# Kernel tuning notes

Measured on AMD Instinct MI355X. Metric: run time of the kernel, lower is better.

The kernel has to match this reference:

```python
import jax, jax.numpy as jnp
import numpy as np
import math

B, S, D = 4, 4096, 1024
H = 16
HD = D // H          # head_dim = 64
M = 256              # nb_features (random projection dim)


def _orthogonal_gaussian(key, m, d):
    # FAVOR+ orthogonal random features: blocks of d orthogonal rows,
    # each row rescaled to a chi-distributed norm (norm of a d-dim gaussian).
    n_blocks = int(math.ceil(m / d))
    keys = jax.random.split(key, n_blocks + 1)
    blocks = []
    for i in range(n_blocks):
        g = jax.random.normal(keys[i], (d, d), dtype=jnp.float32)
        q, _ = jnp.linalg.qr(g)
        blocks.append(q.T)
    W = jnp.concatenate(blocks, axis=0)[:m]  # [m, d]
    norms = jnp.linalg.norm(
        jax.random.normal(keys[-1], (m, d), dtype=jnp.float32), axis=1, keepdims=True)
    return W * norms


def _softmax_kernel(x, proj, is_query, eps=1e-4):
    # x: [b,h,s,d]; proj: [m,d]. Standard FAVOR+ positive softmax features.
    d = x.shape[-1]
    ratio = proj.shape[0] ** -0.5
    x = x * (d ** -0.25)
    u = jnp.einsum('bhsd,md->bhsm', x, proj)  # projection
    diag = 0.5 * jnp.sum(x * x, axis=-1, keepdims=True)  # [b,h,s,1]
    if is_query:
        stab = jnp.max(u, axis=-1, keepdims=True)
    else:
        stab = jnp.max(u, axis=(-1, -2), keepdims=True)
    return ratio * (jnp.exp(u - diag - stab) + eps)


def performer_attention(Q, K, V, mask, proj):
    # Q,K,V: [b,h,s,d], mask: [b,s]
    scale = HD ** -0.25
    m4 = mask[:, None, :, None]
    Qs = Q * scale
    Ks = K * scale * m4
    Vs = V * m4
    q_prime = _softmax_kernel(Qs, proj, is_query=True)   # [b,h,s,m]
    k_prime = _softmax_kernel(Ks, proj, is_query=False)  # [b,h,s,m]
    # linear attention: O(s*m*d)
    kv = jnp.einsum('bhsm,bhsd->bhmd', k_prime, Vs)      # [b,h,m,d]
    z = 1.0 / (jnp.einsum('bhsm,bhm->bhs', q_prime, jnp.sum(k_prime, axis=2)) + 1e-6)
    out = jnp.einsum('bhsm,bhmd->bhsd', q_prime, kv) * z[..., None]
    return out


def setup_inputs() -> dict:
    key = jax.random.key(0)
    ks = jax.random.split(key, 9)
    X = jax.random.normal(ks[0], (B, S, D), dtype=jnp.float32)
    mask = jnp.ones((B, S), dtype=jnp.float32)
    s = D ** -0.5
    Wq = jax.random.normal(ks[1], (D, D), dtype=jnp.float32) * s
    bq = jnp.zeros((D,), dtype=jnp.float32)
    Wk = jax.random.normal(ks[2], (D, D), dtype=jnp.float32) * s
    bk = jnp.zeros((D,), dtype=jnp.float32)
    Wv = jax.random.normal(ks[3], (D, D), dtype=jnp.float32) * s
    bv = jnp.zeros((D,), dtype=jnp.float32)
    proj = _orthogonal_gaussian(ks[4], M, HD)
    return {"X": X, "mask": mask, "Wq": Wq, "bq": bq, "Wk": Wk, "bk": bk,
            "Wv": Wv, "bv": bv, "proj": proj}


def _split_heads(x):
    b, s, _ = x.shape
    return x.reshape(b, s, H, HD).transpose(0, 2, 1, 3)


def reference(X, mask, Wq, bq, Wk, bk, Wv, bv, proj):
    Q = _split_heads(X @ Wq + bq)
    K = _split_heads(X @ Wk + bk)
    V = _split_heads(X @ Wv + bv)
    attn = performer_attention(Q, K, V, mask, proj)  # [b,h,s,hd]
    out = attn.transpose(0, 2, 1, 3).reshape(B, S, D)
    return out
```

## Files before the change

### kernel.cpp

```cpp
#include <hip/hip_runtime.h>
#include <stdint.h>

#define DEVI static __device__ __forceinline__

typedef unsigned short u16;
typedef unsigned int u32;
typedef __attribute__((ext_vector_type(8))) short short8;
typedef __attribute__((ext_vector_type(4))) float f32x4;
typedef __attribute__((ext_vector_type(4))) unsigned short ushort4_t;

#define BB 4
#define SS 4096
#define DD 1024
#define HH 16
#define HDD 64
#define MM 256
#define BHN 64

DEVI u16 f2bf(float f) {
    u32 u = __float_as_uint(f);
    u += 0x7fffu + ((u >> 16) & 1u);
    return (u16)(u >> 16);
}
DEVI float bf2f(u16 h) { return __uint_as_float(((u32)h) << 16); }
DEVI u32 fenc(float f) {
    u32 u = __float_as_uint(f);
    return (u & 0x80000000u) ? ~u : (u | 0x80000000u);
}
DEVI float fdec(u32 k) {
    u32 u = (k & 0x80000000u) ? (k & 0x7fffffffu) : ~k;
    return __uint_as_float(u);
}

typedef __attribute__((address_space(1))) const unsigned int as1_u32;
typedef __attribute__((address_space(3))) unsigned int as3_u32;
DEVI void load_lds16(const void* g, void* lds) {
    __builtin_amdgcn_global_load_lds((as1_u32*)g, (as3_u32*)lds, 16, 0, 0);
}


__global__ void conv_bf16(const float* __restrict__ src, u16* __restrict__ dst, int n4) {
    int i = blockIdx.x * 256 + threadIdx.x;
    if (i < n4) {
        float4 v = reinterpret_cast<const float4*>(src)[i];
        ushort4_t o = { f2bf(v.x), f2bf(v.y), f2bf(v.z), f2bf(v.w) };
        reinterpret_cast<ushort4_t*>(dst)[i] = o;
    }
}

__global__ void conv_w(const float* __restrict__ Wq, const float* __restrict__ Wk,
                       const float* __restrict__ Wv, u16* __restrict__ Wt) {
    __shared__ float tile[64][65];
    const int jt = blockIdx.x, kt = blockIdx.y;
    const float* src = (jt < 16) ? Wq : (jt < 32) ? Wk : Wv;
    const int j0 = (jt & 15) * 64, k0 = kt * 64;
    const int t = threadIdx.x;
    for (int i = 0; i < 16; ++i) {
        int lin = t + i * 256;
        int kl = lin >> 6, jl = lin & 63;
        tile[kl][jl] = src[(size_t)(k0 + kl) * DD + j0 + jl];
    }
    __syncthreads();
    const int jg0 = jt * 64;
    for (int i = 0; i < 16; ++i) {
        int lin = t + i * 256;
        int jl = lin >> 6, kl = lin & 63;
        Wt[(size_t)(jg0 + jl) * DD + k0 + kl] = f2bf(tile[kl][jl]);
    }
}

__global__ __launch_bounds__(512, 2) void gemm1_k32(
    const u16* __restrict__ Xbf, const u16* __restrict__ Wt,
    const float* __restrict__ bq, const float* __restrict__ bk, const float* __restrict__ bv,
    const float* __restrict__ mask,
    u16* __restrict__ Qh, u16* __restrict__ Kh, u16* __restrict__ Vt,
    float* __restrict__ dq, float* __restrict__ dk)
{
    extern __shared__ __align__(16) char smem[];
    const int tid = threadIdx.x, l = tid & 63, wv = tid >> 6;
    const int wm = wv >> 2, wn = wv & 3;
    const int bid = blockIdx.x;
    const int xcd = bid & 7, i6 = bid >> 3;
    const int bx = xcd * 8 + i6 / 12, by = i6 % 12;
    const int row0 = bx * 256, col0 = by * 256;

    int sA[2];
#pragma unroll
    for (int j = 0; j < 2; ++j) {
        const int o = j * 8192 + tid * 16;
        const int R = o >> 7;
        const int logpos = (o & 127) ^ ((R & 7) << 4);
        const int r = 2 * R + (logpos >> 6);
        const int c8 = (logpos >> 4) & 3;
        sA[j] = r * DD + c8 * 8;
    }
    const size_t xbase = (size_t)row0 * DD;
    const size_t wbase = (size_t)col0 * DD;

    #define ABUF(b) ((char*)smem + (b) * 16384)
    #define BBUF(b) ((char*)smem + 65536 + (b) * 16384)
    #define STA(b, kt, j) load_lds16(Xbf + xbase + (kt) * 32 + sA[j], ABUF(b) + (j) * 8192 + wv * 1024)
    #define STB(b, kt, j) load_lds16(Wt + wbase + (kt) * 32 + sA[j], BBUF(b) + (j) * 8192 + wv * 1024)

#pragma unroll
    for (int t = 0; t < 3; ++t) { STA(t, t, 0); STA(t, t, 1); STB(t, t, 0); STB(t, t, 1); }
    asm volatile("s_waitcnt vmcnt(8)" ::: "memory");
    __builtin_amdgcn_s_barrier();
    __builtin_amdgcn_sched_barrier(0);

    f32x4 acc[8][4] = {};
    const int hl = (l & 15) >> 1;
    const int xorc = hl << 4;
    const int pa = ((wm * 64 + hl) * 128 + (l & 1) * 64 + (l >> 4) * 16) ^ xorc;
    const int pb = ((wn * 32 + hl) * 128 + (l & 1) * 64 + (l >> 4) * 16) ^ xorc;

    for (int kt = 0; kt < 32; ++kt) {
        const int p = kt & 3, pn = (kt + 3) & 3;
        const bool more = (kt + 3) < 32;
        short8 bfr[4];
#pragma unroll
        for (int q = 0; q < 4; ++q) {
            if (more) {
                if (q == 0)      STA(pn, kt + 3, 0);
                else if (q == 1) STA(pn, kt + 3, 1);
                else if (q == 2) STB(pn, kt + 3, 0);
                else             STB(pn, kt + 3, 1);
            }
            if (q == 0) {
#pragma unroll
                for (int nf = 0; nf < 4; ++nf)
                    bfr[nf] = *(const short8*)(BBUF(p) + pb + nf * 1024);
            }
            short8 a[2];
#pragma unroll
            for (int i = 0; i < 2; ++i)
                a[i] = *(const short8*)(ABUF(p) + pa + (q * 2 + i) * 1024);
            __builtin_amdgcn_s_setprio(1);
#pragma unroll
            for (int i = 0; i < 2; ++i)
#pragma unroll
                for (int nf = 0; nf < 4; ++nf)
                    acc[q * 2 + i][nf] = __builtin_amdgcn_mfma_f32_16x16x32_bf16(a[i], bfr[nf], acc[q * 2 + i][nf], 0, 0, 0);
            __builtin_amdgcn_s_setprio(0);
        }
        if (kt < 31) {
            if (kt + 3 < 32)      asm volatile("s_waitcnt vmcnt(8)" ::: "memory");
            else if (kt + 2 < 32) asm volatile("s_waitcnt vmcnt(4)" ::: "memory");
            else                  asm volatile("s_waitcnt vmcnt(0)" ::: "memory");
            __builtin_amdgcn_s_barrier();
            __builtin_amdgcn_sched_barrier(0);
        }
    }

    const int region = by >> 2;
    const int h = ((by & 3) << 2) + wn;
    const int rg = row0 + wm * 128;
    const int b = rg >> 12;
    const int sb = rg & 4095;
    const size_t bh = (size_t)(b * HH + h);
    const int dd = l & 15;
    const int jbase = ((by & 3) << 8) + wn * 64;

    if (region == 0) {
        float bias[4];
#pragma unroll
        for (int nf = 0; nf < 4; ++nf) bias[nf] = bq[jbase + nf * 16 + dd];
#pragma unroll
        for (int mf = 0; mf < 8; ++mf) {
            float ds4[4];
#pragma unroll
            for (int g = 0; g < 4; ++g) {
                const int s = sb + mf * 16 + ((l >> 4) << 2) + g;
                float dsum = 0.f;
#pragma unroll
                for (int nf = 0; nf < 4; ++nf) {
                    u16 hv = f2bf((acc[mf][nf][g] + bias[nf]) * 0.125f);
                    Qh[(bh * SS + s) * HDD + nf * 16 + dd] = hv;
                    float fv = bf2f(hv);
                    dsum += fv * fv;
                }
                dsum += __shfl_xor(dsum, 1);
                dsum += __shfl_xor(dsum, 2);
                dsum += __shfl_xor(dsum, 4);
                dsum += __shfl_xor(dsum, 8);
                ds4[g] = 0.5f * dsum;
            }
            if (dd == 0)
                *(float4*)(dq + bh * SS + sb + mf * 16 + ((l >> 4) << 2)) =
                    make_float4(ds4[0], ds4[1], ds4[2], ds4[3]);
        }
    } else if (region == 1) {
        float bias[4];
#pragma unroll
        for (int nf = 0; nf < 4; ++nf) bias[nf] = bk[jbase + nf * 16 + dd];
#pragma unroll
        for (int mf = 0; mf < 8; ++mf) {
            float ds4[4];
#pragma unroll
            for (int g = 0; g < 4; ++g) {
                const int s = sb + mf * 16 + ((l >> 4) << 2) + g;
                const float m = mask[b * SS + s];
                float dsum = 0.f;
#pragma unroll
                for (int nf = 0; nf < 4; ++nf) {
                    u16 hv = f2bf((acc[mf][nf][g] + bias[nf]) * m * 0.125f);
                    Kh[(bh * SS + s) * HDD + nf * 16 + dd] = hv;
                    float fv = bf2f(hv);
                    dsum += fv * fv;
                }
                dsum += __shfl_xor(dsum, 1);
                dsum += __shfl_xor(dsum, 2);
                dsum += __shfl_xor(dsum, 4);
                dsum += __shfl_xor(dsum, 8);
                ds4[g] = 0.5f * dsum;
            }
            if (dd == 0)
                *(float4*)(dk + bh * SS + sb + mf * 16 + ((l >> 4) << 2)) =
                    make_float4(ds4[0], ds4[1], ds4[2], ds4[3]);
        }
    } else {
        float bias[4];
#pragma unroll
        for (int nf = 0; nf < 4; ++nf) bias[nf] = bv[jbase + nf * 16 + dd];
#pragma unroll
        for (int mf = 0; mf < 8; ++mf) {
            const int s0 = sb + mf * 16 + ((l >> 4) << 2);
#pragma unroll
            for (int nf = 0; nf < 4; ++nf) {
                ushort4_t pk;
#pragma unroll
                for (int g = 0; g < 4; ++g) {
                    const float m = mask[b * SS + s0 + g];
                    pk[g] = f2bf((acc[mf][nf][g] + bias[nf]) * m);
                }
                *(ushort4_t*)(Vt + (bh * HDD + nf * 16 + dd) * SS + s0) = pk;
            }
        }
    }
    #undef ABUF
    #undef BBUF
    #undef STA
    #undef STB
}

__global__ __launch_bounds__(256, 2) void stab_kernel(
    const u16* __restrict__ Kh, const u16* __restrict__ projb, u32* __restrict__ stabkey)
{
    __shared__ __align__(16) u16 Klds[64 * 64];
    __shared__ float red4[4];
    const int tid = threadIdx.x, l = tid & 63, wv = tid >> 6;
    const int rt = blockIdx.x, bh = blockIdx.y;
    short8 pb[4][2];
#pragma unroll
    for (int nf = 0; nf < 4; ++nf)
#pragma unroll
        for (int ks = 0; ks < 2; ++ks)
            pb[nf][ks] = *(const short8*)(projb + (wv * 64 + nf * 16 + (l & 15)) * HDD + ks * 32 + (l >> 4) * 8);
    const size_t sbase = (size_t)bh * SS + rt * 64;
#pragma unroll
    for (int c = 0; c < 2; ++c) {
        const int rb = wv * 16 + c * 8;
        const int r = rb + (l >> 3);
        load_lds16(Kh + (sbase + r) * HDD + (((l & 7) ^ (r & 7)) * 8), (char*)Klds + rb * 128);
    }
    __syncthreads();
    float mx = -3.0e38f;
#pragma unroll
    for (int sf = 0; sf < 4; ++sf) {
        const int s = sf * 16 + (l & 15);
        f32x4 u4[4] = {};
#pragma unroll
        for (int ks = 0; ks < 2; ++ks) {
            short8 ak = *(const short8*)((const char*)Klds + s * 128 + ((ks * 64 + (l >> 4) * 16) ^ ((s & 7) << 4)));
#pragma unroll
            for (int nf = 0; nf < 4; ++nf)
                u4[nf] = __builtin_amdgcn_mfma_f32_16x16x32_bf16(ak, pb[nf][ks], u4[nf], 0, 0, 0);
        }
#pragma unroll
        for (int nf = 0; nf < 4; ++nf)
#pragma unroll
            for (int g = 0; g < 4; ++g) mx = fmaxf(mx, u4[nf][g]);
    }
#pragma unroll
    for (int o = 1; o < 64; o <<= 1) mx = fmaxf(mx, __shfl_xor(mx, o));
    if (l == 0) red4[wv] = mx;
    __syncthreads();
    if (tid == 0) {
        float m2 = fmaxf(fmaxf(red4[0], red4[1]), fmaxf(red4[2], red4[3]));
        atomicMax(stabkey + bh, fenc(m2));
    }
}

__global__ __launch_bounds__(256, 2) void kv_fused(
    const u16* __restrict__ Kh, const u16* __restrict__ Vt,
    const u16* __restrict__ projb, const float* __restrict__ dk,
    const u32* __restrict__ stabkey,
    float* __restrict__ kv_part, float* __restrict__ ksum_part)
{
    __shared__ __align__(16) u16 Klds[64 * 64];
    __shared__ __align__(16) u16 Vlds[64 * 64];
    __shared__ __align__(16) u16 Kp[256 * 64];
    const int tid = threadIdx.x, l = tid & 63, wv = tid >> 6;
    const int ck = blockIdx.x, bh = blockIdx.y;
    const float stab = fdec(stabkey[bh]);
    short8 pb[4][2];
#pragma unroll
    for (int nf = 0; nf < 4; ++nf)
#pragma unroll
        for (int ks = 0; ks < 2; ++ks)
            pb[nf][ks] = *(const short8*)(projb + (wv * 64 + nf * 16 + (l & 15)) * HDD + ks * 32 + (l >> 4) * 8);
    f32x4 acc[4][4] = {};
    float ksc[4] = {0.f, 0.f, 0.f, 0.f};
    const size_t sbase = (size_t)bh * SS + ck * 512;
    for (int it = 0; it < 8; ++it) {
        const int s0 = it * 64;
#pragma unroll
        for (int c = 0; c < 2; ++c) {
            const int rb = wv * 16 + c * 8;
            const int r = rb + (l >> 3);
            const int sc = ((l & 7) ^ (r & 7)) * 8;
            load_lds16(Kh + (sbase + s0 + r) * HDD + sc, (char*)Klds + rb * 128);
            load_lds16(Vt + ((size_t)bh * HDD + r) * SS + ck * 512 + s0 + sc, (char*)Vlds + rb * 128);
        }
        __syncthreads();
#pragma unroll
        for (int sf = 0; sf < 4; ++sf) {
            const int s = sf * 16 + (l & 15);
            f32x4 u4[4] = {};
#pragma unroll
            for (int ks = 0; ks < 2; ++ks) {
                short8 ak = *(const short8*)((const char*)Klds + s * 128 + ((ks * 64 + (l >> 4) * 16) ^ ((s & 7) << 4)));
#pragma unroll
                for (int nf = 0; nf < 4; ++nf)
                    u4[nf] = __builtin_amdgcn_mfma_f32_16x16x32_bf16(ak, pb[nf][ks], u4[nf], 0, 0, 0);
            }
            const int srow = sf * 16 + (l >> 4) * 4;
            const float4 dkv = *(const float4*)(dk + sbase + s0 + srow);
#pragma unroll
            for (int nf = 0; nf < 4; ++nf) {
                const int m = wv * 64 + nf * 16 + (l & 15);
                u16 h0 = f2bf(0.0625f * (__expf(u4[nf][0] - dkv.x - stab) + 1e-4f));
                u16 h1 = f2bf(0.0625f * (__expf(u4[nf][1] - dkv.y - stab) + 1e-4f));
                u16 h2 = f2bf(0.0625f * (__expf(u4[nf][2] - dkv.z - stab) + 1e-4f));
                u16 h3 = f2bf(0.0625f * (__expf(u4[nf][3] - dkv.w - stab) + 1e-4f));
                ksc[nf] += bf2f(h0) + bf2f(h1) + bf2f(h2) + bf2f(h3);
                uint2 w; w.x = (u32)h0 | ((u32)h1 << 16); w.y = (u32)h2 | ((u32)h3 << 16);
                *(uint2*)((char*)Kp + m * 128 + ((srow * 2) ^ ((m & 7) << 4))) = w;
            }
        }
#pragma unroll
        for (int ks = 0; ks < 2; ++ks) {
            short8 am[4], bv8[4];
#pragma unroll
            for (int mf = 0; mf < 4; ++mf) {
                const int m = wv * 64 + mf * 16 + (l & 15);
                am[mf] = *(const short8*)((const char*)Kp + m * 128 + ((ks * 64 + (l >> 4) * 16) ^ ((m & 7) << 4)));
            }
#pragma unroll
            for (int nf = 0; nf < 4; ++nf) {
                const int d = nf * 16 + (l & 15);
                bv8[nf] = *(const short8*)((const char*)Vlds + d * 128 + ((ks * 64 + (l >> 4) * 16) ^ ((d & 7) << 4)));
            }
#pragma unroll
            for (int mf = 0; mf < 4; ++mf)
#pragma unroll
                for (int nf = 0; nf < 4; ++nf)
                    acc[mf][nf] = __builtin_amdgcn_mfma_f32_16x16x32_bf16(am[mf], bv8[nf], acc[mf][nf], 0, 0, 0);
        }
        __syncthreads();
    }
    const size_t pbase = (size_t)ck * BHN + bh;
#pragma unroll
    for (int nf = 0; nf < 4; ++nf) {
        float v = ksc[nf];
        v += __shfl_xor(v, 16);
        v += __shfl_xor(v, 32);
        if (l < 16) ksum_part[pbase * MM + wv * 64 + nf * 16 + l] = v;
    }
#pragma unroll
    for (int mf = 0; mf < 4; ++mf)
#pragma unroll
        for (int nf = 0; nf < 4; ++nf)
            *(f32x4*)(kv_part + (pbase * HDD + nf * 16 + (l & 15)) * MM + wv * 64 + mf * 16 + (l >> 4) * 4) = acc[mf][nf];
}

__global__ void reduceB2(const float* __restrict__ kv_part, const float* __restrict__ ksum_part,
                         u16* __restrict__ Bmat) {
    const int bh = blockIdx.x, n = blockIdx.y, t = threadIdx.x;
    float s = 0.f;
    if (n < 64) {
#pragma unroll
        for (int ck = 0; ck < 8; ++ck) s += kv_part[(((size_t)ck * BHN + bh) * HDD + n) * MM + t];
    } else if (n == 64) {
#pragma unroll
        for (int ck = 0; ck < 8; ++ck) s += ksum_part[((size_t)ck * BHN + bh) * MM + t];
    }
    Bmat[((size_t)bh * 80 + n) * MM + t] = (n <= 64) ? f2bf(s) : (u16)0;
}

__global__ __launch_bounds__(256, 2) void out_fused(
    const u16* __restrict__ Qh, const u16* __restrict__ projb,
    const float* __restrict__ dq, const u16* __restrict__ Bmat,
    float* __restrict__ out)
{
    __shared__ __align__(16) u16 Blds[80 * 256];
    __shared__ __align__(16) u16 Qlds[32 * 64];
    __shared__ __align__(16) u16 qlds[32 * 256];
    __shared__ float red[4][32];
    const int tid = threadIdx.x, l = tid & 63, wv = tid >> 6;
    const int rt = blockIdx.x, bh = blockIdx.y;
#pragma unroll
    for (int c = 0; c < 10; ++c) {
        const int r = (wv * 10 + c) * 2 + (l >> 5);
        load_lds16(Bmat + (size_t)bh * 20480 + r * 256 + (((l & 31) ^ (r & 7)) * 8),
                   (char*)Blds + (wv * 10 + c) * 1024);
    }
    const size_t srowbase = (size_t)bh * SS + rt * 32;
    {
        const int rb = wv * 8;
        const int r = rb + (l >> 3);
        load_lds16(Qh + (srowbase + r) * HDD + (((l & 7) ^ (r & 7)) * 8), (char*)Qlds + rb * 128);
    }
    short8 pa[4][2];
#pragma unroll
    for (int mf = 0; mf < 4; ++mf)
#pragma unroll
        for (int ks = 0; ks < 2; ++ks)
            pa[mf][ks] = *(const short8*)(projb + (wv * 64 + mf * 16 + (l & 15)) * HDD + ks * 32 + (l >> 4) * 8);
    __syncthreads();
    f32x4 u[4][2] = {};
#pragma unroll
    for (int ks = 0; ks < 2; ++ks) {
        short8 bq8[2];
#pragma unroll
        for (int nf = 0; nf < 2; ++nf) {
            const int s = nf * 16 + (l & 15);
            bq8[nf] = *(const short8*)((const char*)Qlds + s * 128 + ((ks * 64 + (l >> 4) * 16) ^ ((s & 7) << 4)));
        }
#pragma unroll
        for (int mf = 0; mf < 4; ++mf)
#pragma unroll
            for (int nf = 0; nf < 2; ++nf)
                u[mf][nf] = __builtin_amdgcn_mfma_f32_16x16x32_bf16(pa[mf][ks], bq8[nf], u[mf][nf], 0, 0, 0);
    }
#pragma unroll
    for (int nf = 0; nf < 2; ++nf) {
        float v = -3.0e38f;
#pragma unroll
        for (int mf = 0; mf < 4; ++mf)
#pragma unroll
            for (int g = 0; g < 4; ++g) v = fmaxf(v, u[mf][nf][g]);
        v = fmaxf(v, __shfl_xor(v, 16));
        v = fmaxf(v, __shfl_xor(v, 32));
        if ((l >> 4) == 0) red[wv][nf * 16 + l] = v;
    }
    __syncthreads();
#pragma unroll
    for (int nf = 0; nf < 2; ++nf) {
        const int s = nf * 16 + (l & 15);
        const float mx = fmaxf(fmaxf(red[0][s], red[1][s]), fmaxf(red[2][s], red[3][s]));
        const float dg = dq[srowbase + s];
#pragma unroll
        for (int mf = 0; mf < 4; ++mf) {
            u16 h0 = f2bf(0.0625f * (__expf(u[mf][nf][0] - dg - mx) + 1e-4f));
            u16 h1 = f2bf(0.0625f * (__expf(u[mf][nf][1] - dg - mx) + 1e-4f));
            u16 h2 = f2bf(0.0625f * (__expf(u[mf][nf][2] - dg - mx) + 1e-4f));
            u16 h3 = f2bf(0.0625f * (__expf(u[mf][nf][3] - dg - mx) + 1e-4f));
            uint2 w; w.x = (u32)h0 | ((u32)h1 << 16); w.y = (u32)h2 | ((u32)h3 << 16);
            const int mb = (wv * 64 + mf * 16 + (l >> 4) * 4) * 2;
            *(uint2*)((char*)qlds + s * 512 + (mb ^ ((s & 7) << 4))) = w;
        }
    }
    __syncthreads();
    f32x4 acc[2][2] = {};
    for (int kt = 0; kt < 8; ++kt) {
        short8 aq[2], bb[2];
#pragma unroll
        for (int mf = 0; mf < 2; ++mf) {
            const int s = mf * 16 + (l & 15);
            aq[mf] = *(const short8*)((const char*)qlds + s * 512 + ((kt * 64 + (l >> 4) * 16) ^ ((s & 7) << 4)));
        }
        {
            const int n0 = wv * 16 + (l & 15);
            bb[0] = *(const short8*)((const char*)Blds + n0 * 512 + ((kt * 64 + (l >> 4) * 16) ^ ((n0 & 7) << 4)));
            const int n1 = 64 + (l & 15);
            bb[1] = *(const short8*)((const char*)Blds + n1 * 512 + ((kt * 64 + (l >> 4) * 16) ^ ((n1 & 7) << 4)));
        }
#pragma unroll
        for (int mf = 0; mf < 2; ++mf)
#pragma unroll
            for (int nf = 0; nf < 2; ++nf)
                acc[mf][nf] = __builtin_amdgcn_mfma_f32_16x16x32_bf16(aq[mf], bb[nf], acc[mf][nf], 0, 0, 0);
    }
    const int b = bh >> 4, h = bh & 15;
#pragma unroll
    for (int mf = 0; mf < 2; ++mf) {
#pragma unroll
        for (int g = 0; g < 4; ++g) {
            const float den = __shfl(acc[mf][1][g], (l & 48));
            const float z = 1.0f / (den + 1e-6f);
            const int s = rt * 32 + mf * 16 + (l >> 4) * 4 + g;
            out[((size_t)b * SS + s) * DD + h * HDD + wv * 16 + (l & 15)] = acc[mf][0][g] * z;
        }
    }
}

extern "C" void kernel_launch(void* const* d_in, const int* in_sizes, int n_in,
                              void* d_out, int out_size, void* d_ws, size_t ws_size,
                              hipStream_t stream)
{
    const float* X    = (const float*)d_in[0];
    const float* mask = (const float*)d_in[1];
    const float* Wq   = (const float*)d_in[2];
    const float* bq   = (const float*)d_in[3];
    const float* Wk   = (const float*)d_in[4];
    const float* bk   = (const float*)d_in[5];
    const float* Wv   = (const float*)d_in[6];
    const float* bv   = (const float*)d_in[7];
    const float* proj = (const float*)d_in[8];
    float* out = (float*)d_out;

    char* p = (char*)d_ws;
    u16* Xbf = (u16*)p;
    float* kv_part = (float*)p; p += 33554432;
    u16* Wt = (u16*)p;    p += 6291456;
    u16* projb = (u16*)p; p += 32768;
    u16* Qh = (u16*)p;    p += 33554432;
    u16* Kh = (u16*)p;    p += 33554432;
    u16* Vt = (u16*)p;    p += 33554432;
    float* dq = (float*)p; p += 1048576;
    float* dk = (float*)p; p += 1048576;
    u32* stabkey = (u32*)p; p += 256;
    float* ksum_part = (float*)p; p += 524288;
    u16* Bmat = (u16*)p;  p += 2621440;
    if (ws_size < 145785088ull) return;

    hipFuncSetAttribute((const void*)gemm1_k32, hipFuncAttributeMaxDynamicSharedMemorySize, 131072);

    hipMemsetAsync(stabkey, 0, 256, stream);
    conv_bf16<<<16384, 256, 0, stream>>>(X, Xbf, 4194304);
    conv_w<<<dim3(48, 16), 256, 0, stream>>>(Wq, Wk, Wv, Wt);
    conv_bf16<<<16, 256, 0, stream>>>(proj, projb, 4096);
    gemm1_k32<<<768, 512, 131072, stream>>>(Xbf, Wt, bq, bk, bv, mask, Qh, Kh, Vt, dq, dk);
    stab_kernel<<<dim3(64, 64), 256, 0, stream>>>(Kh, projb, stabkey);
    kv_fused<<<dim3(8, 64), 256, 0, stream>>>(Kh, Vt, projb, dk, stabkey, kv_part, ksum_part);
    reduceB2<<<dim3(64, 80), 256, 0, stream>>>(kv_part, ksum_part, Bmat);
    out_fused<<<dim3(128, 64), 256, 0, stream>>>(Qh, projb, dq, Bmat, out);
}
```

Before: 305.1 us.

## Restructure gemm main loop into two phases, triple-buffer kv loads, retile output kernel

The projection GEMM loop is reorganised into two half-phases per k-step, each issuing its global-to-LDS prefetch, loading fragments, then running a barrier-fenced MFMA burst. kv_fused moves to dynamic shared memory with a three-deep K/V buffer ring so the next chunk's loads overlap compute, which adds a barrier in the middle of each iteration. out_fused doubles its row tile to 64, halving the grid, and reads the B matrix straight from global memory instead of staging it in LDS. These aim to hide memory latency and cut redundant B loads, at the cost of more barriers and possibly lower occupancy.

Result: no change. 299.3 us (-1.9%).

```diff
diff --git a/kernel.cpp b/kernel.cpp
--- a/kernel.cpp
+++ b/kernel.cpp
@@ -69,7 +69,7 @@
     }
 }
 
-__global__ __launch_bounds__(512, 2) void gemm1_k32(
+__global__ __launch_bounds__(512, 2) void gemm1_2ph(
     const u16* __restrict__ Xbf, const u16* __restrict__ Wt,
     const float* __restrict__ bq, const float* __restrict__ bk, const float* __restrict__ bv,
     const float* __restrict__ mask,
@@ -117,39 +117,45 @@
     for (int kt = 0; kt < 32; ++kt) {
         const int p = kt & 3, pn = (kt + 3) & 3;
         const bool more = (kt + 3) < 32;
-        short8 bfr[4];
-#pragma unroll
-        for (int q = 0; q < 4; ++q) {
-            if (more) {
-                if (q == 0)      STA(pn, kt + 3, 0);
-                else if (q == 1) STA(pn, kt + 3, 1);
-                else if (q == 2) STB(pn, kt + 3, 0);
-                else             STB(pn, kt + 3, 1);
-            }
-            if (q == 0) {
-#pragma unroll
-                for (int nf = 0; nf < 4; ++nf)
-                    bfr[nf] = *(const short8*)(BBUF(p) + pb + nf * 1024);
-            }
-            short8 a[2];
-#pragma unroll
-            for (int i = 0; i < 2; ++i)
-                a[i] = *(const short8*)(ABUF(p) + pa + (q * 2 + i) * 1024);
-            __builtin_amdgcn_s_setprio(1);
-#pragma unroll
-            for (int i = 0; i < 2; ++i)
-#pragma unroll
-                for (int nf = 0; nf < 4; ++nf)
-                    acc[q * 2 + i][nf] = __builtin_amdgcn_mfma_f32_16x16x32_bf16(a[i], bfr[nf], acc[q * 2 + i][nf], 0, 0, 0);
-            __builtin_amdgcn_s_setprio(0);
-        }
-        if (kt < 31) {
-            if (kt + 3 < 32)      asm volatile("s_waitcnt vmcnt(8)" ::: "memory");
-            else if (kt + 2 < 32) asm volatile("s_waitcnt vmcnt(4)" ::: "memory");
-            else                  asm volatile("s_waitcnt vmcnt(0)" ::: "memory");
-            __builtin_amdgcn_s_barrier();
-            __builtin_amdgcn_sched_barrier(0);
-        }
+        short8 bfr[4], a0[4], a1[4];
+        if (more) { STA(pn, kt + 3, 0); STA(pn, kt + 3, 1); }
+#pragma unroll
+        for (int nf = 0; nf < 4; ++nf)
+            bfr[nf] = *(const short8*)(BBUF(p) + pb + nf * 1024);
+#pragma unroll
+        for (int i = 0; i < 4; ++i)
+            a0[i] = *(const short8*)(ABUF(p) + pa + i * 1024);
+        __builtin_amdgcn_s_barrier();
+        asm volatile("s_waitcnt lgkmcnt(0)" ::: "memory");
+        __builtin_amdgcn_sched_barrier(0);
+        __builtin_amdgcn_s_setprio(1);
+#pragma unroll
+        for (int i = 0; i < 4; ++i)
+#pragma unroll
+            for (int nf = 0; nf < 4; ++nf)
+                acc[i][nf] = __builtin_amdgcn_mfma_f32_16x16x32_bf16(a0[i], bfr[nf], acc[i][nf], 0, 0, 0);
+        __builtin_amdgcn_s_setprio(0);
+        __builtin_amdgcn_sched_barrier(0);
+        __builtin_amdgcn_s_barrier();
+        if (more) { STB(pn, kt + 3, 0); STB(pn, kt + 3, 1); }
+#pragma unroll
+        for (int i = 0; i < 4; ++i)
+            a1[i] = *(const short8*)(ABUF(p) + pa + (4 + i) * 1024);
+        __builtin_amdgcn_s_barrier();
+        asm volatile("s_waitcnt lgkmcnt(0)" ::: "memory");
+        __builtin_amdgcn_sched_barrier(0);
+        __builtin_amdgcn_s_setprio(1);
+#pragma unroll
+        for (int i = 0; i < 4; ++i)
+#pragma unroll
+            for (int nf = 0; nf < 4; ++nf)
+                acc[4 + i][nf] = __builtin_amdgcn_mfma_f32_16x16x32_bf16(a1[i], bfr[nf], acc[4 + i][nf], 0, 0, 0);
+        __builtin_amdgcn_s_setprio(0);
+        __builtin_amdgcn_sched_barrier(0);
+        if (kt + 3 < 32)      asm volatile("s_waitcnt vmcnt(8)" ::: "memory");
+        else if (kt + 2 < 32) asm volatile("s_waitcnt vmcnt(4)" ::: "memory");
+        else                  asm volatile("s_waitcnt vmcnt(0)" ::: "memory");
+        __builtin_amdgcn_s_barrier();
     }
 
     const int region = by >> 2;
@@ -297,9 +303,10 @@
     const u32* __restrict__ stabkey,
     float* __restrict__ kv_part, float* __restrict__ ksum_part)
 {
-    __shared__ __align__(16) u16 Klds[64 * 64];
-    __shared__ __align__(16) u16 Vlds[64 * 64];
-    __shared__ __align__(16) u16 Kp[256 * 64];
+    extern __shared__ __align__(16) char ksm[];
+    #define KLDS(b) ((char*)ksm + (b) * 8192)
+    #define VLDS(b) ((char*)ksm + 24576 + (b) * 8192)
+    u16* Kp = (u16*)((char*)ksm + 49152);
     const int tid = threadIdx.x, l = tid & 63, wv = tid >> 6;
     const int ck = blockIdx.x, bh = blockIdx.y;
     const float stab = fdec(stabkey[bh]);
@@ -312,24 +319,37 @@
     f32x4 acc[4][4] = {};
     float ksc[4] = {0.f, 0.f, 0.f, 0.f};
     const size_t sbase = (size_t)bh * SS + ck * 512;
+
+    #define KVSTAGE(buf, it8) do { \
+        const int s0_ = (it8) * 64; \
+        _Pragma("unroll") \
+        for (int c = 0; c < 2; ++c) { \
+            const int rb = wv * 16 + c * 8; \
+            const int r = rb + (l >> 3); \
+            const int sc = ((l & 7) ^ (r & 7)) * 8; \
+            load_lds16(Kh + (sbase + s0_ + r) * HDD + sc, KLDS(buf) + rb * 128); \
+            load_lds16(Vt + ((size_t)bh * HDD + r) * SS + ck * 512 + s0_ + sc, VLDS(buf) + rb * 128); \
+        } \
+    } while (0)
+
+    KVSTAGE(0, 0);
     for (int it = 0; it < 8; ++it) {
+        const int bs = it % 3;
+        if (it + 1 < 8) {
+            KVSTAGE((it + 1) % 3, it + 1);
+            asm volatile("s_waitcnt vmcnt(4)" ::: "memory");
+        } else {
+            asm volatile("s_waitcnt vmcnt(0)" ::: "memory");
+        }
+        __syncthreads();
         const int s0 = it * 64;
-#pragma unroll
-        for (int c = 0; c < 2; ++c) {
-            const int rb = wv * 16 + c * 8;
-            const int r = rb + (l >> 3);
-            const int sc = ((l & 7) ^ (r & 7)) * 8;
-            load_lds16(Kh + (sbase + s0 + r) * HDD + sc, (char*)Klds + rb * 128);
-            load_lds16(Vt + ((size_t)bh * HDD + r) * SS + ck * 512 + s0 + sc, (char*)Vlds + rb * 128);
-        }
-        __syncthreads();
 #pragma unroll
         for (int sf = 0; sf < 4; ++sf) {
             const int s = sf * 16 + (l & 15);
             f32x4 u4[4] = {};
 #pragma unroll
             for (int ks = 0; ks < 2; ++ks) {
-                short8 ak = *(const short8*)((const char*)Klds + s * 128 + ((ks * 64 + (l >> 4) * 16) ^ ((s & 7) << 4)));
+                short8 ak = *(const short8*)(KLDS(bs) + s * 128 + ((ks * 64 + (l >> 4) * 16) ^ ((s & 7) << 4)));
 #pragma unroll
                 for (int nf = 0; nf < 4; ++nf)
                     u4[nf] = __builtin_amdgcn_mfma_f32_16x16x32_bf16(ak, pb[nf][ks], u4[nf], 0, 0, 0);
@@ -348,6 +368,7 @@
                 *(uint2*)((char*)Kp + m * 128 + ((srow * 2) ^ ((m & 7) << 4))) = w;
             }
         }
+        __syncthreads();
 #pragma unroll
         for (int ks = 0; ks < 2; ++ks) {
             short8 am[4], bv8[4];
@@ -359,7 +380,7 @@
 #pragma unroll
             for (int nf = 0; nf < 4; ++nf) {
                 const int d = nf * 16 + (l & 15);
-                bv8[nf] = *(const short8*)((const char*)Vlds + d * 128 + ((ks * 64 + (l >> 4) * 16) ^ ((d & 7) << 4)));
+                bv8[nf] = *(const short8*)(VLDS(bs) + d * 128 + ((ks * 64 + (l >> 4) * 16) ^ ((d & 7) << 4)));
             }
 #pragma unroll
             for (int mf = 0; mf < 4; ++mf)
@@ -367,7 +388,6 @@
                 for (int nf = 0; nf < 4; ++nf)
                     acc[mf][nf] = __builtin_amdgcn_mfma_f32_16x16x32_bf16(am[mf], bv8[nf], acc[mf][nf], 0, 0, 0);
         }
-        __syncthreads();
     }
     const size_t pbase = (size_t)ck * BHN + bh;
 #pragma unroll
@@ -382,6 +402,9 @@
 #pragma unroll
         for (int nf = 0; nf < 4; ++nf)
             *(f32x4*)(kv_part + (pbase * HDD + nf * 16 + (l & 15)) * MM + wv * 64 + mf * 16 + (l >> 4) * 4) = acc[mf][nf];
+    #undef KLDS
+    #undef VLDS
+    #undef KVSTAGE
 }
 
 __global__ void reduceB2(const float* __restrict__ kv_part, const float* __restrict__ ksum_part,
@@ -398,26 +421,20 @@
     Bmat[((size_t)bh * 80 + n) * MM + t] = (n <= 64) ? f2bf(s) : (u16)0;
 }
 
-__global__ __launch_bounds__(256, 2) void out_fused(
+__global__ __launch_bounds__(256) void out_fused(
     const u16* __restrict__ Qh, const u16* __restrict__ projb,
     const float* __restrict__ dq, const u16* __restrict__ Bmat,
     float* __restrict__ out)
 {
-    __shared__ __align__(16) u16 Blds[80 * 256];
-    __shared__ __align__(16) u16 Qlds[32 * 64];
-    __shared__ __align__(16) u16 qlds[32 * 256];
-    __shared__ float red[4][32];
+    __shared__ __align__(16) u16 Qlds[64 * 64];
+    __shared__ __align__(16) u16 qlds[64 * 256];
+    __shared__ float red[4][64];
     const int tid = threadIdx.x, l = tid & 63, wv = tid >> 6;
     const int rt = blockIdx.x, bh = blockIdx.y;
-#pragma unroll
-    for (int c = 0; c < 10; ++c) {
-        const int r = (wv * 10 + c) * 2 + (l >> 5);
-        load_lds16(Bmat + (size_t)bh * 20480 + r * 256 + (((l & 31) ^ (r & 7)) * 8),
-                   (char*)Blds + (wv * 10 + c) * 1024);
-    }
-    const size_t srowbase = (size_t)bh * SS + rt * 32;
-    {
-        const int rb = wv * 8;
+    const size_t srowbase = (size_t)bh * SS + rt * 64;
+#pragma unroll
+    for (int c = 0; c < 2; ++c) {
+        const int rb = wv * 16 + c * 8;
         const int r = rb + (l >> 3);
         load_lds16(Qh + (srowbase + r) * HDD + (((l & 7) ^ (r & 7)) * 8), (char*)Qlds + rb * 128);
     }
@@ -428,23 +445,23 @@
         for (int ks = 0; ks < 2; ++ks)
             pa[mf][ks] = *(const short8*)(projb + (wv * 64 + mf * 16 + (l & 15)) * HDD + ks * 32 + (l >> 4) * 8);
     __syncthreads();
-    f32x4 u[4][2] = {};
+    f32x4 u[4][4] = {};
 #pragma unroll
     for (int ks = 0; ks < 2; ++ks) {
-        short8 bq8[2];
-#pragma unroll
-        for (int nf = 0; nf < 2; ++nf) {
+        short8 bq8[4];
+#pragma unroll
+        for (int nf = 0; nf < 4; ++nf) {
             const int s = nf * 16 + (l & 15);
             bq8[nf] = *(const short8*)((const char*)Qlds + s * 128 + ((ks * 64 + (l >> 4) * 16) ^ ((s & 7) << 4)));
         }
 #pragma unroll
         for (int mf = 0; mf < 4; ++mf)
 #pragma unroll
-            for (int nf = 0; nf < 2; ++nf)
+            for (int nf = 0; nf < 4; ++nf)
                 u[mf][nf] = __builtin_amdgcn_mfma_f32_16x16x32_bf16(pa[mf][ks], bq8[nf], u[mf][nf], 0, 0, 0);
     }
 #pragma unroll
-    for (int nf = 0; nf < 2; ++nf) {
+    for (int nf = 0; nf < 4; ++nf) {
         float v = -3.0e38f;
 #pragma unroll
         for (int mf = 0; mf < 4; ++mf)
@@ -456,7 +473,7 @@
     }
     __syncthreads();
 #pragma unroll
-    for (int nf = 0; nf < 2; ++nf) {
+    for (int nf = 0; nf < 4; ++nf) {
         const int s = nf * 16 + (l & 15);
         const float mx = fmaxf(fmaxf(red[0][s], red[1][s]), fmaxf(red[2][s], red[3][s]));
         const float dg = dq[srowbase + s];
@@ -472,34 +489,32 @@
         }
     }
     __syncthreads();
-    f32x4 acc[2][2] = {};
+    const u16* bbase = Bmat + (size_t)bh * 20480;
+    f32x4 acc[4][2] = {};
+#pragma unroll
     for (int kt = 0; kt < 8; ++kt) {
-        short8 aq[2], bb[2];
-#pragma unroll
-        for (int mf = 0; mf < 2; ++mf) {
+        short8 aq[4], bb[2];
+#pragma unroll
+        for (int mf = 0; mf < 4; ++mf) {
             const int s = mf * 16 + (l & 15);
             aq[mf] = *(const short8*)((const char*)qlds + s * 512 + ((kt * 64 + (l >> 4) * 16) ^ ((s & 7) << 4)));
         }
-        {
-            const int n0 = wv * 16 + (l & 15);
-            bb[0] = *(const short8*)((const char*)Blds + n0 * 512 + ((kt * 64 + (l >> 4) * 16) ^ ((n0 & 7) << 4)));
-            const int n1 = 64 + (l & 15);
-            bb[1] = *(const short8*)((const char*)Blds + n1 * 512 + ((kt * 64 + (l >> 4) * 16) ^ ((n1 & 7) << 4)));
-        }
-#pragma unroll
-        for (int mf = 0; mf < 2; ++mf)
+        bb[0] = *(const short8*)(bbase + (wv * 16 + (l & 15)) * 256 + kt * 32 + (l >> 4) * 8);
+        bb[1] = *(const short8*)(bbase + (64 + (l & 15)) * 256 + kt * 32 + (l >> 4) * 8);
+#pragma unroll
+        for (int mf = 0; mf < 4; ++mf)
 #pragma unroll
             for (int nf = 0; nf < 2; ++nf)
                 acc[mf][nf] = __builtin_amdgcn_mfma_f32_16x16x32_bf16(aq[mf], bb[nf], acc[mf][nf], 0, 0, 0);
     }
     const int b = bh >> 4, h = bh & 15;
 #pragma unroll
-    for (int mf = 0; mf < 2; ++mf) {
+    for (int mf = 0; mf < 4; ++mf) {
 #pragma unroll
         for (int g = 0; g < 4; ++g) {
             const float den = __shfl(acc[mf][1][g], (l & 48));
             const float z = 1.0f / (den + 1e-6f);
-            const int s = rt * 32 + mf * 16 + (l >> 4) * 4 + g;
+            const int s = rt * 64 + mf * 16 + (l >> 4) * 4 + g;
             out[((size_t)b * SS + s) * DD + h * HDD + wv * 16 + (l & 15)] = acc[mf][0][g] * z;
         }
     }
@@ -535,15 +550,16 @@
     u16* Bmat = (u16*)p;  p += 2621440;
     if (ws_size < 145785088ull) return;
 
-    hipFuncSetAttribute((const void*)gemm1_k32, hipFuncAttributeMaxDynamicSharedMemorySize, 131072);
+    hipFuncSetAttribute((const void*)gemm1_2ph, hipFuncAttributeMaxDynamicSharedMemorySize, 131072);
+    hipFuncSetAttribute((const void*)kv_fused, hipFuncAttributeMaxDynamicSharedMemorySize, 81920);
 
     hipMemsetAsync(stabkey, 0, 256, stream);
     conv_bf16<<<16384, 256, 0, stream>>>(X, Xbf, 4194304);
     conv_w<<<dim3(48, 16), 256, 0, stream>>>(Wq, Wk, Wv, Wt);
     conv_bf16<<<16, 256, 0, stream>>>(proj, projb, 4096);
-    gemm1_k32<<<768, 512, 131072, stream>>>(Xbf, Wt, bq, bk, bv, mask, Qh, Kh, Vt, dq, dk);
+    gemm1_2ph<<<768, 512, 131072, stream>>>(Xbf, Wt, bq, bk, bv, mask, Qh, Kh, Vt, dq, dk);
     stab_kernel<<<dim3(64, 64), 256, 0, stream>>>(Kh, projb, stabkey);
-    kv_fused<<<dim3(8, 64), 256, 0, stream>>>(Kh, Vt, projb, dk, stabkey, kv_part, ksum_part);
+    kv_fused<<<dim3(8, 64), 256, 81920, stream>>>(Kh, Vt, projb, dk, stabkey, kv_part, ksum_part);
     reduceB2<<<dim3(64, 80), 256, 0, stream>>>(kv_part, ksum_part, Bmat);
-    out_fused<<<dim3(128, 64), 256, 0, stream>>>(Qh, projb, dq, Bmat, out);
-}
+    out_fused<<<dim3(64, 64), 256, 0, stream>>>(Qh, projb, dq, Bmat, out);
+}
```
